# Kernel optimization log

Measured on AMD Instinct MI355X. Metric: run time of the kernel, lower is better.

## Reference

```python
import jax, jax.numpy as jnp
import numpy as np

B, C, H, W = 8, 96, 56, 56
N = H * W
K = 9
COUT = 2 * C  # 192


def setup_inputs() -> dict:
    key = jax.random.key(0)
    ks = jax.random.split(key, 12)
    s = 0.05
    inp = {
        "x": jax.random.normal(ks[0], (B, C, H, W), jnp.float32),
        "kmap_w": jax.random.normal(ks[1], (C, 500), jnp.float32) * s,
        "kmap_b": jnp.zeros((500,), jnp.float32),
        "kfc_w": jax.random.normal(ks[2], (500, 64), jnp.float32) * s,
        "kfc_b": jnp.zeros((64,), jnp.float32),
        "kmu_w": jax.random.normal(ks[3], (64, 32), jnp.float32) * s,
        "kmu_b": jnp.zeros((32,), jnp.float32),
        "kdec_w": jax.random.normal(ks[4], (32, K), jnp.float32) * s,
        "kdec_b": jnp.zeros((K,), jnp.float32),
        "ec1_w": jax.random.normal(ks[5], (2 * C, C), jnp.float32) * s,
        "ec1_b": jnp.zeros((C,), jnp.float32),
        "ec2_w": jax.random.normal(ks[6], (2 * C, C), jnp.float32) * s,
        "ec2_b": jnp.zeros((C,), jnp.float32),
        "fc_w": jax.random.normal(ks[7], (C, COUT), jnp.float32) * s,
        "fc_b": jnp.zeros((COUT,), jnp.float32),
        "io_w": jax.random.normal(ks[8], (C, COUT), jnp.float32) * s,
        "io_b": jnp.zeros((COUT,), jnp.float32),
        "up_w": jax.random.normal(ks[9], (2 * COUT, COUT), jnp.float32) * s,
        "up_b": jnp.zeros((COUT,), jnp.float32),
    }
    return inp


def reference(x, kmap_w, kmap_b, kfc_w, kfc_b, kmu_w, kmu_b, kdec_w, kdec_b,
              ec1_w, ec1_b, ec2_w, ec2_b, fc_w, fc_b, io_w, io_b, up_w, up_b):
    b, c, h, w = x.shape
    n = h * w
    xf = x.reshape(b, c, n).transpose(0, 2, 1)  # [B, N, C]

    # ---- dense kNN graph (dilation=1, deterministic) ----
    sq = jnp.sum(xf * xf, axis=-1)  # [B, N]
    dist = sq[:, :, None] - 2.0 * jnp.einsum('bnc,bmc->bnm', xf, xf) + sq[:, None, :]
    _, nn_idx = jax.lax.top_k(-dist, K)  # [B, N, K] local neighbor indices

    nodes = xf.reshape(b * n, c)  # flat node features

    # ---- VAE-like K predictor -> per-node kept-degree (non-differentiable) ----
    hK = nodes @ kmap_w + kmap_b
    hK = jax.nn.relu(hK @ kfc_w + kfc_b)
    mu = hK @ kmu_w + kmu_b
    logits = mu @ kdec_w + kdec_b  # [B*N, K]
    k_int = jnp.argmax(logits, axis=1)  # in [0, K-1]

    # edge mask: keep first k_int[i] of node i's K edges
    edge_mask = (jnp.arange(K)[None, :] < k_int[:, None]).reshape(-1)  # [B*N*K]
    emask = edge_mask.astype(nodes.dtype)[:, None]

    # flatten edges with per-batch node offsets (local -> global indices)
    offs = (jnp.arange(b) * n)[:, None, None]
    src = (nn_idx + offs).reshape(-1)              # x_j
    dst = jnp.repeat(jnp.arange(b * n), K)         # x_i (center)

    def edge_conv(feat, wgt, bias):
        xi = feat[dst]
        xj = feat[src]
        msg = jnp.concatenate([xi, xj - xi], axis=-1) @ wgt + bias
        msg = msg * emask  # pruned edges contribute 0 to 'add' aggregation
        return jax.ops.segment_sum(msg, dst, num_segments=b * n)

    h1 = jax.nn.relu(edge_conv(nodes, ec1_w, ec1_b))
    h2 = edge_conv(h1, ec2_w, ec2_b)
    agg = h2 @ fc_w + fc_b                 # EdgeAgg output [B*N, COUT]

    xio = nodes @ io_w + io_b              # inOutFC
    upd = jax.nn.relu(jnp.concatenate([xio, agg], axis=-1) @ up_w + up_b)

    out = upd.reshape(b, n, 2 * c).transpose(0, 2, 1).reshape(b, 2 * c, h, w)
    return out
```

## Files before the change

### kernel.cpp

```cpp
#include <hip/hip_runtime.h>

#define NODES 25088
#define NB 8
#define NPB 3136
#define C 96
#define KNN 9
#define COUT 192
#define MSPLIT 4
#define T12 12
#define NCAND (MSPLIT * T12)

typedef float f32x4 __attribute__((ext_vector_type(4)));
typedef float f32x16 __attribute__((ext_vector_type(16)));
typedef short s16x8 __attribute__((ext_vector_type(8)));

__device__ __forceinline__ unsigned short f2bf(float x) {
  unsigned u = __float_as_uint(x);
  return (unsigned short)((u + 0x7fffu + ((u >> 16) & 1u)) >> 16);
}
__device__ __forceinline__ float bf2f(unsigned short h) {
  return __uint_as_float(((unsigned)h) << 16);
}

__global__ __launch_bounds__(256) void txsq_kernel(
    const float* __restrict__ x, float* __restrict__ xf, float* __restrict__ sq,
    unsigned short* __restrict__ xh, unsigned short* __restrict__ xl) {
  __shared__ float t[96][33];
  int tid = threadIdx.x;
  int b = blockIdx.y;
  int n0 = blockIdx.x * 32;
  const float* xb = x + (size_t)b * C * NPB;
  int tn = tid & 31, tc = tid >> 5;
#pragma unroll
  for (int i = 0; i < 12; i++) {
    int c = tc + i * 8;
    t[c][tn] = xb[(size_t)c * NPB + n0 + tn];
  }
  __syncthreads();
#pragma unroll
  for (int k = 0; k < 3; k++) {
    int it = tid + k * 256;
    int nl = it / 24, c4 = it % 24;
    int node = b * NPB + n0 + nl;
    float4 v;
    v.x = t[4 * c4 + 0][nl];
    v.y = t[4 * c4 + 1][nl];
    v.z = t[4 * c4 + 2][nl];
    v.w = t[4 * c4 + 3][nl];
    ushort4 h, l;
    h.x = f2bf(v.x); l.x = f2bf(v.x - bf2f(h.x));
    h.y = f2bf(v.y); l.y = f2bf(v.y - bf2f(h.y));
    h.z = f2bf(v.z); l.z = f2bf(v.z - bf2f(h.z));
    h.w = f2bf(v.w); l.w = f2bf(v.w - bf2f(h.w));
    ((float4*)(xf + (size_t)node * C))[c4] = v;
    ((ushort4*)(xh + (size_t)node * C))[c4] = h;
    ((ushort4*)(xl + (size_t)node * C))[c4] = l;
  }
  if (tid < 32) {
    int node = b * NPB + n0 + tid;
    float s = 0.f;
#pragma unroll
    for (int i = 0; i < 24; i++) {
      float4 v;
      v.x = t[4 * i + 0][tid];
      v.y = t[4 * i + 1][tid];
      v.z = t[4 * i + 2][tid];
      v.w = t[4 * i + 3][tid];
      s += v.x * v.x + v.y * v.y + v.z * v.z + v.w * v.w;
    }
    sq[node] = s;
  }
}

__global__ void fold_all_kernel(
    const float* __restrict__ kmap_w, const float* __restrict__ kmap_b,
    const float* __restrict__ kfc_w, const float* __restrict__ kfc_b,
    const float* __restrict__ kmu_w, const float* __restrict__ kmu_b,
    const float* __restrict__ kdec_w, const float* __restrict__ kdec_b,
    const float* __restrict__ ec1_w, const float* __restrict__ ec2_w,
    const float* __restrict__ io_w, const float* __restrict__ io_b,
    const float* __restrict__ fc_w, const float* __restrict__ fc_b,
    const float* __restrict__ up_w, const float* __restrict__ up_b,
    float* __restrict__ WkP, float* __restrict__ bkP, float* __restrict__ WdP,
    float* __restrict__ bdP, float* __restrict__ bPf,
    unsigned short* __restrict__ B1h, unsigned short* __restrict__ B1l,
    unsigned short* __restrict__ B2h, unsigned short* __restrict__ B2l,
    unsigned short* __restrict__ BFh, unsigned short* __restrict__ BFl) {
  __shared__ float sh[4][64];
  int bid = blockIdx.x, tid = threadIdx.x;
  int tx = tid & 63, ty = tid >> 6;
  if (bid < 96) {
    int m = bid;
    float acc = 0.f;
    for (int k = ty; k < 500; k += 4) acc += kmap_w[m * 500 + k] * kfc_w[k * 64 + tx];
    sh[ty][tx] = acc;
    __syncthreads();
    if (ty == 0) WkP[m * 64 + tx] = sh[0][tx] + sh[1][tx] + sh[2][tx] + sh[3][tx];
  } else if (bid == 96) {
    float acc = 0.f;
    for (int k = ty; k < 500; k += 4) acc += kmap_b[k] * kfc_w[k * 64 + tx];
    sh[ty][tx] = acc;
    __syncthreads();
    if (ty == 0) bkP[tx] = sh[0][tx] + sh[1][tx] + sh[2][tx] + sh[3][tx] + kfc_b[tx];
  } else if (bid < 161) {
    int m = bid - 97;
    float acc = 0.f;
    if (tx < 9) {
      for (int k = ty; k < 32; k += 4) acc += kmu_w[m * 32 + k] * kdec_w[k * 9 + tx];
    }
    sh[ty][tx] = acc;
    __syncthreads();
    if (ty == 0 && tx < 9) WdP[m * 9 + tx] = sh[0][tx] + sh[1][tx] + sh[2][tx] + sh[3][tx];
  } else if (bid == 161) {
    float acc = 0.f;
    if (tx < 9) {
      for (int k = ty; k < 32; k += 4) acc += kmu_b[k] * kdec_w[k * 9 + tx];
    }
    sh[ty][tx] = acc;
    __syncthreads();
    if (ty == 0 && tx < 9) bdP[tx] = sh[0][tx] + sh[1][tx] + sh[2][tx] + sh[3][tx] + kdec_b[tx];
  } else if (bid < 234) {
    int t = (bid - 162) * 256 + tid;
    int n = t / 192, k = t % 192;
    float v = ec1_w[(size_t)k * 96 + n];
    if (k < 96) v -= ec1_w[(size_t)(k + 96) * 96 + n];
    unsigned short h = f2bf(v);
    B1h[t] = h;
    B1l[t] = f2bf(v - bf2f(h));
  } else if (bid < 306) {
    int t = (bid - 234) * 256 + tid;
    int n = t / 192, k = t % 192;
    float v = ec2_w[(size_t)k * 96 + n];
    if (k < 96) v -= ec2_w[(size_t)(k + 96) * 96 + n];
    unsigned short h = f2bf(v);
    B2h[t] = h;
    B2l[t] = f2bf(v - bf2f(h));
  } else if (bid < 594) {
    int r = bid - 306;
    int m = r / 3, n = (r % 3) * 64 + tx;
    float acc = 0.f;
    for (int k = ty; k < 192; k += 4) acc += io_w[m * 192 + k] * up_w[(size_t)k * 192 + n];
    sh[ty][tx] = acc;
    __syncthreads();
    if (ty == 0) {
      float v = sh[0][tx] + sh[1][tx] + sh[2][tx] + sh[3][tx];
      unsigned short h = f2bf(v);
      BFh[(size_t)n * 192 + m] = h;
      BFl[(size_t)n * 192 + m] = f2bf(v - bf2f(h));
    }
  } else if (bid < 882) {
    int r = bid - 594;
    int m = r / 3, n = (r % 3) * 64 + tx;
    float acc = 0.f;
    for (int k = ty; k < 192; k += 4)
      acc += fc_w[m * 192 + k] * up_w[(size_t)(192 + k) * 192 + n];
    sh[ty][tx] = acc;
    __syncthreads();
    if (ty == 0) {
      float v = sh[0][tx] + sh[1][tx] + sh[2][tx] + sh[3][tx];
      unsigned short h = f2bf(v);
      BFh[(size_t)n * 192 + 96 + m] = h;
      BFl[(size_t)n * 192 + 96 + m] = f2bf(v - bf2f(h));
    }
  } else {
    if (tid < 192) {
      float acc = up_b[tid];
      for (int k = 0; k < 192; k++) {
        acc += io_b[k] * up_w[k * 192 + tid];
        acc += fc_b[k] * up_w[(192 + k) * 192 + tid];
      }
      bPf[tid] = acc;
    }
  }
}

__global__ __launch_bounds__(256) void gemmhead_kernel(
    const float* __restrict__ A0, const float* __restrict__ B,
    const float* __restrict__ bias, const float* __restrict__ WdP,
    const float* __restrict__ bdP, int* __restrict__ kint,
    float* __restrict__ rs) {
  __shared__ float As[16][68];
  __shared__ float Bs[16][68];
  __shared__ float hs[64][68];
  __shared__ float wd[576];
  __shared__ float bd[9];
  int tid = threadIdx.x;
  int tx = tid & 15, ty = tid >> 4;
  int row0 = blockIdx.x * 64;
  for (int f = tid; f < 576; f += 256) wd[f] = WdP[f];
  if (tid < 9) bd[tid] = bdP[tid];
  float acc[4][4] = {};
  int ai = tid >> 2;
  int ak = (tid & 3) * 4;
  int bk = tid >> 4;
  int bj = (tid & 15) * 4;

  for (int k0 = 0; k0 < 96; k0 += 16) {
    {
      int r = row0 + ai;
      float4 v = *(const float4*)(A0 + (size_t)r * 96 + k0 + ak);
      As[ak + 0][ai] = v.x;
      As[ak + 1][ai] = v.y;
      As[ak + 2][ai] = v.z;
      As[ak + 3][ai] = v.w;
    }
    {
      int kg = k0 + bk;
      float4 v = *(const float4*)(B + (size_t)kg * 64 + bj);
      *(float4*)&Bs[bk][bj] = v;
    }
    __syncthreads();
#pragma unroll
    for (int kk = 0; kk < 16; kk++) {
      float4 av = *(const float4*)&As[kk][ty * 4];
      float4 bv = *(const float4*)&Bs[kk][tx * 4];
      acc[0][0] += av.x * bv.x; acc[0][1] += av.x * bv.y; acc[0][2] += av.x * bv.z; acc[0][3] += av.x * bv.w;
      acc[1][0] += av.y * bv.x; acc[1][1] += av.y * bv.y; acc[1][2] += av.y * bv.z; acc[1][3] += av.y * bv.w;
      acc[2][0] += av.z * bv.x; acc[2][1] += av.z * bv.y; acc[2][2] += av.z * bv.z; acc[2][3] += av.z * bv.w;
      acc[3][0] += av.w * bv.x; acc[3][1] += av.w * bv.y; acc[3][2] += av.w * bv.z; acc[3][3] += av.w * bv.w;
    }
    __syncthreads();
  }
#pragma unroll
  for (int ii = 0; ii < 4; ii++) {
#pragma unroll
    for (int jj = 0; jj < 4; jj++) {
      int j = tx * 4 + jj;
      hs[ty * 4 + ii][j] = fmaxf(acc[ii][jj] + bias[j], 0.f);
    }
  }
  __syncthreads();
  if (tid < 64) {
    int node = row0 + tid;
    const float4* hp = (const float4*)hs[tid];
    float4 h[16];
#pragma unroll
    for (int i = 0; i < 16; i++) h[i] = hp[i];
    float best = -3.4e38f;
    int bi = 0;
#pragma unroll
    for (int n = 0; n < 9; n++) {
      float a = bd[n];
#pragma unroll
      for (int k = 0; k < 16; k++) {
        float4 hv = h[k];
        a += hv.x * wd[(4 * k + 0) * 9 + n] + hv.y * wd[(4 * k + 1) * 9 + n] +
             hv.z * wd[(4 * k + 2) * 9 + n] + hv.w * wd[(4 * k + 3) * 9 + n];
      }
      if (a > best) { best = a; bi = n; }
    }
    kint[node] = bi;
    rs[node] = (float)bi;
  }
}

__device__ __forceinline__ void ce(float& a, float& b) {
  float lo = fminf(a, b);
  b = fmaxf(a, b);
  a = lo;
}

__device__ __forceinline__ void sort16(float* s) {
  ce(s[0], s[1]); ce(s[2], s[3]); ce(s[0], s[2]); ce(s[1], s[3]); ce(s[1], s[2]);
  ce(s[4], s[5]); ce(s[6], s[7]); ce(s[4], s[6]); ce(s[5], s[7]); ce(s[5], s[6]);
  ce(s[0], s[4]); ce(s[1], s[5]); ce(s[2], s[6]); ce(s[3], s[7]);
  ce(s[2], s[4]); ce(s[3], s[5]);
  ce(s[1], s[2]); ce(s[3], s[4]); ce(s[5], s[6]);
  ce(s[8], s[9]); ce(s[10], s[11]); ce(s[8], s[10]); ce(s[9], s[11]); ce(s[9], s[10]);
  ce(s[12], s[13]); ce(s[14], s[15]); ce(s[12], s[14]); ce(s[13], s[15]); ce(s[13], s[14]);
  ce(s[8], s[12]); ce(s[9], s[13]); ce(s[10], s[14]); ce(s[11], s[15]);
  ce(s[10], s[12]); ce(s[11], s[13]);
  ce(s[9], s[10]); ce(s[11], s[12]); ce(s[13], s[14]);
  ce(s[0], s[8]); ce(s[1], s[9]); ce(s[2], s[10]); ce(s[3], s[11]);
  ce(s[4], s[12]); ce(s[5], s[13]); ce(s[6], s[14]); ce(s[7], s[15]);
  ce(s[4], s[8]); ce(s[5], s[9]); ce(s[6], s[10]); ce(s[7], s[11]);
  ce(s[2], s[4]); ce(s[3], s[5]); ce(s[6], s[8]); ce(s[7], s[9]);
  ce(s[10], s[12]); ce(s[11], s[13]);
  ce(s[1], s[2]); ce(s[3], s[4]); ce(s[5], s[6]); ce(s[7], s[8]);
  ce(s[9], s[10]); ce(s[11], s[12]); ce(s[13], s[14]);
}

__device__ __forceinline__ void bmerge12(float* fd, const float* s) {
  float L[12];
#pragma unroll
  for (int i = 0; i < 12; i++) L[i] = fminf(fd[i], s[11 - i]);
  ce(L[0], L[8]); ce(L[1], L[9]); ce(L[2], L[10]); ce(L[3], L[11]);
  ce(L[4], L[8]); ce(L[5], L[9]); ce(L[6], L[10]); ce(L[7], L[11]);
  ce(L[0], L[2]); ce(L[1], L[3]); ce(L[4], L[6]); ce(L[5], L[7]);
  ce(L[8], L[10]); ce(L[9], L[11]);
  ce(L[0], L[1]); ce(L[2], L[3]); ce(L[4], L[5]); ce(L[6], L[7]);
  ce(L[8], L[9]); ce(L[10], L[11]);
#pragma unroll
  for (int i = 0; i < 12; i++) fd[i] = L[i];
}

__global__ __launch_bounds__(256) void knn_mfma_kernel(
    const unsigned short* __restrict__ xh, const unsigned short* __restrict__ xl,
    const float* __restrict__ sq, int* __restrict__ pk_i) {
  __shared__ __align__(16) float smem_f[6784];
  unsigned short* mhA = (unsigned short*)smem_f;
  unsigned short* mhB = (unsigned short*)(smem_f + 3328);
  float* sqsA = smem_f + 6656;
  float* sqsB = smem_f + 6720;
  int tid = threadIdx.x;
  int lane = tid & 63, wv = tid >> 6;
  int wm = wv >> 1, wq = wv & 1;
  int bid = blockIdx.x;
  int b = bid & 7;
  int r = bid >> 3;
  int q0 = (r % 49) * 64;
  int z = r / 49;
  int bbase = b * NPB;
  int t0 = (z * 49) / MSPLIT, t1 = ((z + 1) * 49) / MSPLIT;

  int koff = (lane >> 5) * 8;
  int qrow = bbase + q0 + wq * 32 + (lane & 31);
  s16x8 bqh[6], bql[6];
  {
    const unsigned short* ph = xh + (size_t)qrow * 96 + koff;
    const unsigned short* pl = xl + (size_t)qrow * 96 + koff;
#pragma unroll
    for (int kc = 0; kc < 6; kc++) {
      bqh[kc] = *(const s16x8*)(ph + kc * 16);
      bql[kc] = *(const s16x8*)(pl + kc * 16);
    }
  }
  float sqr = sq[qrow];

  float fd[12];
#pragma unroll
  for (int k = 0; k < 12; k++) fd[k] = 3.4e38f;

  int srow = tid >> 1;
  int tloc = srow >> 6;
  int rrow = srow & 63;
  int sseg = (tid & 1) * 48;
  int soff = rrow * 104 + sseg;
  unsigned short* mhd = tloc ? mhB : mhA;

  s16x8 st[6];
  float stq = 0.f;
  {
    int tA = t0 + tloc;
    int ts = (tA < t1) ? tA : (t1 - 1);
    const unsigned short* gh = xh + (size_t)(bbase + ts * 64 + rrow) * 96 + sseg;
#pragma unroll
    for (int i = 0; i < 6; i++) st[i] = *(const s16x8*)(gh + i * 8);
    if (tid < 128) {
      int tq = t0 + (tid >> 6);
      int tqs = (tq < t1) ? tq : (t1 - 1);
      stq = sq[bbase + tqs * 64 + (tid & 63)];
    }
  }

  int sqbase = wm * 32 + 4 * (lane >> 5);
  int mrow = wm * 32 + (lane & 31);
  int np = (t1 - t0 + 1) >> 1;

  for (int p = 0; p < np; p++) {
    int ta = t0 + 2 * p, tb = ta + 1;
    __syncthreads();
#pragma unroll
    for (int i = 0; i < 6; i++) *(s16x8*)(mhd + soff + i * 8) = st[i];
    if (tid < 128) ((tid >> 6) ? sqsB : sqsA)[tid & 63] = stq;
    __syncthreads();

    {
      int tn = t0 + 2 * (p + 1) + tloc;
      int ts = (tn < t1) ? tn : (t1 - 1);
      const unsigned short* gh = xh + (size_t)(bbase + ts * 64 + rrow) * 96 + sseg;
#pragma unroll
      for (int i = 0; i < 6; i++) st[i] = *(const s16x8*)(gh + i * 8);
      if (tid < 128) {
        int tq = t0 + 2 * (p + 1) + (tid >> 6);
        int tqs = (tq < t1) ? tq : (t1 - 1);
        stq = sq[bbase + tqs * 64 + (tid & 63)];
      }
    }

    {
      f32x16 acc = (f32x16){0.f, 0.f, 0.f, 0.f, 0.f, 0.f, 0.f, 0.f,
                            0.f, 0.f, 0.f, 0.f, 0.f, 0.f, 0.f, 0.f};
#pragma unroll
      for (int kc = 0; kc < 6; kc++) {
        s16x8 amh = *(const s16x8*)(mhA + mrow * 104 + kc * 16 + koff);
        acc = __builtin_amdgcn_mfma_f32_32x32x16_bf16(amh, bqh[kc], acc, 0, 0, 0);
        acc = __builtin_amdgcn_mfma_f32_32x32x16_bf16(amh, bql[kc], acc, 0, 0, 0);
      }
      f32x4 sm0 = *(const f32x4*)(sqsA + sqbase);
      f32x4 sm1 = *(const f32x4*)(sqsA + sqbase + 8);
      f32x4 sm2 = *(const f32x4*)(sqsA + sqbase + 16);
      f32x4 sm3 = *(const f32x4*)(sqsA + sqbase + 24);
      int lbase = (ta - t0) * 64;
      float cs[16];
#pragma unroll
      for (int reg = 0; reg < 16; reg++) {
        int g = reg >> 2, e = reg & 3;
        float sqm = (g == 0) ? sm0[e] : (g == 1) ? sm1[e] : (g == 2) ? sm2[e] : sm3[e];
        int mloc = wm * 32 + e + 8 * g + 4 * (lane >> 5);
        float d = fmaf(-2.f, acc[reg], sqr + sqm);
        unsigned u = (__float_as_uint(d) & 0xFFFFFC00u) | (unsigned)(lbase + mloc);
        cs[reg] = __uint_as_float(u);
      }
      sort16(cs);
      bmerge12(fd, cs);
    }
    if (tb < t1) {
      f32x16 acc = (f32x16){0.f, 0.f, 0.f, 0.f, 0.f, 0.f, 0.f, 0.f,
                            0.f, 0.f, 0.f, 0.f, 0.f, 0.f, 0.f, 0.f};
#pragma unroll
      for (int kc = 0; kc < 6; kc++) {
        s16x8 amh = *(const s16x8*)(mhB + mrow * 104 + kc * 16 + koff);
        acc = __builtin_amdgcn_mfma_f32_32x32x16_bf16(amh, bqh[kc], acc, 0, 0, 0);
        acc = __builtin_amdgcn_mfma_f32_32x32x16_bf16(amh, bql[kc], acc, 0, 0, 0);
      }
      f32x4 sm0 = *(const f32x4*)(sqsB + sqbase);
      f32x4 sm1 = *(const f32x4*)(sqsB + sqbase + 8);
      f32x4 sm2 = *(const f32x4*)(sqsB + sqbase + 16);
      f32x4 sm3 = *(const f32x4*)(sqsB + sqbase + 24);
      int lbase = (tb - t0) * 64;
      float cs[16];
#pragma unroll
      for (int reg = 0; reg < 16; reg++) {
        int g = reg >> 2, e = reg & 3;
        float sqm = (g == 0) ? sm0[e] : (g == 1) ? sm1[e] : (g == 2) ? sm2[e] : sm3[e];
        int mloc = wm * 32 + e + 8 * g + 4 * (lane >> 5);
        float d = fmaf(-2.f, acc[reg], sqr + sqm);
        unsigned u = (__float_as_uint(d) & 0xFFFFFC00u) | (unsigned)(lbase + mloc);
        cs[reg] = __uint_as_float(u);
      }
      sort16(cs);
      bmerge12(fd, cs);
    }
  }

  __syncthreads();
  float* cd = smem_f;
#pragma unroll
  for (int k = 0; k < 12; k++) cd[(wv * 64 + lane) * 13 + k] = fd[k];
  __syncthreads();
  if (wv == 0) {
    int wva = lane >> 5, ql = lane & 31;
    int ra = wva * 64 + ql, rb = wva * 64 + ql + 32;
    int rc = (wva + 2) * 64 + ql, rd = (wva + 2) * 64 + ql + 32;
    float A[12], B[12];
#pragma unroll
    for (int k = 0; k < 12; k++) { A[k] = cd[ra * 13 + k]; B[k] = cd[rb * 13 + k]; }
    bmerge12(A, B);
    float Cc[12], Dd[12];
#pragma unroll
    for (int k = 0; k < 12; k++) { Cc[k] = cd[rc * 13 + k]; Dd[k] = cd[rd * 13 + k]; }
    bmerge12(Cc, Dd);
    bmerge12(A, Cc);
    size_t base = ((size_t)(bbase + q0 + lane) * MSPLIT + z) * T12;
#pragma unroll
    for (int k = 0; k < T12; k++) {
      int mloc = (int)(__float_as_uint(A[k]) & 0x3FFu) + t0 * 64;
      pk_i[base + k] = bbase + mloc;
    }
  }
}

__global__ __launch_bounds__(256) void rescore_kernel(
    const float* __restrict__ xf, const float* __restrict__ sq,
    const int* __restrict__ pk_i, int* __restrict__ nn) {
  __shared__ float qr[4][96];
  __shared__ float sqq[4];
  int tid = threadIdx.x;
  int qloc = tid >> 6, c = tid & 63;
  int bid = blockIdx.x;
  int qbase = (bid & 7) * NPB + (bid >> 3) * 4;
  for (int f = tid; f < 4 * 96; f += 256)
    qr[f / 96][f % 96] = xf[(size_t)(qbase + f / 96) * 96 + f % 96];
  if (tid < 4) sqq[tid] = sq[qbase + tid];
  __syncthreads();

  int q = qbase + qloc;
  int jv = 0;
  if (c < NCAND) jv = pk_i[(size_t)q * NCAND + c];

  int grp = c >> 3;
  int chunk = c & 7;
  const float4* qp = (const float4*)qr[qloc];
  float4 qv0 = qp[chunk];
  float4 qv1 = qp[chunk + 8];
  float4 qv2 = qp[chunk + 16];

  float dots[6];
#pragma unroll
  for (int it = 0; it < 6; it++) {
    int j = __shfl(jv, it * 8 + grp, 64);
    const float4* mp = (const float4*)(xf + (size_t)j * 96);
    float4 m0 = mp[chunk];
    float4 m1 = mp[chunk + 8];
    float4 m2 = mp[chunk + 16];
    float p = qv0.x * m0.x + qv0.y * m0.y + qv0.z * m0.z + qv0.w * m0.w +
              qv1.x * m1.x + qv1.y * m1.y + qv1.z * m1.z + qv1.w * m1.w +
              qv2.x * m2.x + qv2.y * m2.y + qv2.z * m2.z + qv2.w * m2.w;
    p += __shfl_xor(p, 1, 64);
    p += __shfl_xor(p, 2, 64);
    p += __shfl_xor(p, 4, 64);
    dots[it] = p;
  }

  float g0 = __shfl(dots[0], (c & 7) * 8, 64);
  float g1 = __shfl(dots[1], (c & 7) * 8, 64);
  float g2 = __shfl(dots[2], (c & 7) * 8, 64);
  float g3 = __shfl(dots[3], (c & 7) * 8, 64);
  float g4 = __shfl(dots[4], (c & 7) * 8, 64);
  float g5 = __shfl(dots[5], (c & 7) * 8, 64);
  int itstar = c >> 3;
  float dot = g0;
  dot = (itstar == 1) ? g1 : dot;
  dot = (itstar == 2) ? g2 : dot;
  dot = (itstar == 3) ? g3 : dot;
  dot = (itstar == 4) ? g4 : dot;
  dot = (itstar == 5) ? g5 : dot;

  unsigned long long key = 0xFFFFFFFFFFFFFFFFull;
  if (c < NCAND) {
    float d = (sqq[qloc] - 2.0f * dot) + sq[jv];
    unsigned u = __float_as_uint(d);
    u ^= (u & 0x80000000u) ? 0xFFFFFFFFu : 0x80000000u;
    key = ((unsigned long long)u << 32) | (unsigned)jv;
  }

#pragma unroll
  for (int k = 2; k <= 64; k <<= 1) {
#pragma unroll
    for (int jm = k >> 1; jm >= 1; jm >>= 1) {
      unsigned long long other = __shfl_xor(key, jm, 64);
      bool takeMin = ((c & jm) == 0) == ((c & k) == 0);
      bool sw = (other < key) == takeMin;
      key = sw ? other : key;
    }
  }

  if (c < KNN) {
    nn[(size_t)q * KNN + c] = (int)(unsigned)(key & 0xFFFFFFFFull);
  }
}

// ... 139 lines not shown
    }
    size_t bo = (size_t)n * 192 + c * 16 + koff;
    s16x8 bh = *(const s16x8*)(Bth + bo);
    s16x8 bl = *(const s16x8*)(Btl + bo);
    acc = __builtin_amdgcn_mfma_f32_32x32x16_bf16(ah, bh, acc, 0, 0, 0);
    acc = __builtin_amdgcn_mfma_f32_32x32x16_bf16(al, bh, acc, 0, 0, 0);
    acc = __builtin_amdgcn_mfma_f32_32x32x16_bf16(ah, bl, acc, 0, 0, 0);
  }

  float bn = bL[wv * 32 + nloc];
#pragma unroll
  for (int reg = 0; reg < 16; reg++) {
    int rl = (reg & 3) + 8 * (reg >> 2) + 4 * (lane >> 5);
    tt[wv][nloc][rl] = fmaxf(acc[reg] + bn, 0.f);
  }
  __builtin_amdgcn_s_waitcnt(0);
  int gbase = m0 + nloc;
  int bb = gbase / NPB, nidx = gbase % NPB;
#pragma unroll
  for (int i = 0; i < 16; i++) {
    int nl = 2 * i + (lane >> 5);
    float v = tt[wv][nl][nloc];
    int ng = n0 + wv * 32 + nl;
    out[(size_t)bb * COUT * NPB + (size_t)ng * NPB + nidx] = v;
  }
}

extern "C" void kernel_launch(void* const* d_in, const int* in_sizes, int n_in,
                              void* d_out, int out_size, void* d_ws, size_t ws_size,
                              hipStream_t stream) {
  const float* x      = (const float*)d_in[0];
  const float* kmap_w = (const float*)d_in[1];
  const float* kmap_b = (const float*)d_in[2];
  const float* kfc_w  = (const float*)d_in[3];
  const float* kfc_b  = (const float*)d_in[4];
  const float* kmu_w  = (const float*)d_in[5];
  const float* kmu_b  = (const float*)d_in[6];
  const float* kdec_w = (const float*)d_in[7];
  const float* kdec_b = (const float*)d_in[8];
  const float* ec1_w  = (const float*)d_in[9];
  const float* ec1_b  = (const float*)d_in[10];
  const float* ec2_w  = (const float*)d_in[11];
  const float* ec2_b  = (const float*)d_in[12];
  const float* fc_w   = (const float*)d_in[13];
  const float* fc_b   = (const float*)d_in[14];
  const float* io_w   = (const float*)d_in[15];
  const float* io_b   = (const float*)d_in[16];
  const float* up_w   = (const float*)d_in[17];
  const float* up_b   = (const float*)d_in[18];

  char* ws = (char*)d_ws;
  size_t off = 0;
  auto alloc = [&](size_t bytes) -> void* {
    void* p = ws + off;
    off += (bytes + 255) & ~(size_t)255;
    return p;
  };
  const size_t HBF = (size_t)NODES * C * 2;
  float* xf   = (float*)alloc((size_t)NODES * C * 4);
  float* sqb  = (float*)alloc((size_t)NODES * 4);
  float* rs   = (float*)alloc((size_t)NODES * 4);
  int*   kint = (int*)alloc((size_t)NODES * 4);
  int*   nn   = (int*)alloc((size_t)NODES * KNN * 4);
  unsigned short* xh = (unsigned short*)alloc(HBF);
  unsigned short* xl = (unsigned short*)alloc(HBF);
  char* region = (char*)alloc((size_t)NODES * COUT * 4);
  int*   pk_i   = (int*)region;
  unsigned short* h1h = (unsigned short*)region;
  unsigned short* h1l = (unsigned short*)(region + HBF);
  unsigned short* h2h = (unsigned short*)(region + 2 * HBF);
  unsigned short* h2l = (unsigned short*)(region + 3 * HBF);
  float* WkP = (float*)alloc(96 * 64 * 4);
  float* bkP = (float*)alloc(64 * 4);
  float* WdP = (float*)alloc(64 * 9 * 4);
  float* bdP = (float*)alloc(16 * 4);
  float* bPf = (float*)alloc(192 * 4);
  unsigned short* B1h = (unsigned short*)alloc(96 * 192 * 2);
  unsigned short* B1l = (unsigned short*)alloc(96 * 192 * 2);
  unsigned short* B2h = (unsigned short*)alloc(96 * 192 * 2);
  unsigned short* B2l = (unsigned short*)alloc(96 * 192 * 2);
  unsigned short* BFh = (unsigned short*)alloc(192 * 192 * 2);
  unsigned short* BFl = (unsigned short*)alloc(192 * 192 * 2);

  txsq_kernel<<<dim3(98, 8), 256, 0, stream>>>(x, xf, sqb, xh, xl);

  fold_all_kernel<<<883, 256, 0, stream>>>(
      kmap_w, kmap_b, kfc_w, kfc_b, kmu_w, kmu_b, kdec_w, kdec_b, ec1_w, ec2_w,
      io_w, io_b, fc_w, fc_b, up_w, up_b,
      WkP, bkP, WdP, bdP, bPf, B1h, B1l, B2h, B2l, BFh, BFl);

  gemmhead_kernel<<<392, 256, 0, stream>>>(xf, WkP, bkP, WdP, bdP, kint, rs);

  knn_mfma_kernel<<<1568, 256, 0, stream>>>(xh, xl, sqb, pk_i);
  rescore_kernel<<<6272, 256, 0, stream>>>(xf, sqb, pk_i, nn);

  mfma_ec_fused_kernel<<<784, 192, 0, stream>>>(
      xh, xl, xf, (const unsigned short*)nullptr, (const unsigned short*)nullptr,
      0, nn, kint, B1h, B1l, rs, ec1_b, 1, h1h, h1l);
  mfma_ec_fused_kernel<<<784, 192, 0, stream>>>(
      h1h, h1l, (const float*)nullptr, h1h, h1l,
      1, nn, kint, B2h, B2l, rs, ec2_b, 0, h2h, h2l);
  mfma_final_kernel<<<dim3(784, 2), 192, 0, stream>>>(xh, xl, h2h, h2l, BFh, BFl,
                                                      bPf, (float*)d_out);
}
```

Measured before the change: 320.0 us.

## Merge independent kernels into two block-dispatched launches to cut launch overhead

Combines the transpose/split kernel with the weight-folding kernel into one launch, and the kNN MFMA kernel with the K-predictor GEMM head into another, choosing the role of each block by its block index. Independent work now runs concurrently within one grid, and two kernel launches and their inter-kernel gaps go away. In exchange, the fused kernels carry the union of shared-memory sizes and register pressure, which may reduce occupancy for the lighter branches.

```diff
diff --git a/kernel.cpp b/kernel.cpp
--- a/kernel.cpp
+++ b/kernel.cpp
@@ -22,57 +22,49 @@
   return __uint_as_float(((unsigned)h) << 16);
 }
 
-__global__ __launch_bounds__(256) void txsq_kernel(
+__device__ __forceinline__ void ce(float& a, float& b) {
+  float lo = fminf(a, b);
+  b = fmaxf(a, b);
+  a = lo;
+}
+
+__device__ __forceinline__ void sort16(float* s) {
+  ce(s[0], s[1]); ce(s[2], s[3]); ce(s[0], s[2]); ce(s[1], s[3]); ce(s[1], s[2]);
+  ce(s[4], s[5]); ce(s[6], s[7]); ce(s[4], s[6]); ce(s[5], s[7]); ce(s[5], s[6]);
+  ce(s[0], s[4]); ce(s[1], s[5]); ce(s[2], s[6]); ce(s[3], s[7]);
+  ce(s[2], s[4]); ce(s[3], s[5]);
+  ce(s[1], s[2]); ce(s[3], s[4]); ce(s[5], s[6]);
+  ce(s[8], s[9]); ce(s[10], s[11]); ce(s[8], s[10]); ce(s[9], s[11]); ce(s[9], s[10]);
+  ce(s[12], s[13]); ce(s[14], s[15]); ce(s[12], s[14]); ce(s[13], s[15]); ce(s[13], s[14]);
+  ce(s[8], s[12]); ce(s[9], s[13]); ce(s[10], s[14]); ce(s[11], s[15]);
+  ce(s[10], s[12]); ce(s[11], s[13]);
+  ce(s[9], s[10]); ce(s[11], s[12]); ce(s[13], s[14]);
+  ce(s[0], s[8]); ce(s[1], s[9]); ce(s[2], s[10]); ce(s[3], s[11]);
+  ce(s[4], s[12]); ce(s[5], s[13]); ce(s[6], s[14]); ce(s[7], s[15]);
+  ce(s[4], s[8]); ce(s[5], s[9]); ce(s[6], s[10]); ce(s[7], s[11]);
+  ce(s[2], s[4]); ce(s[3], s[5]); ce(s[6], s[8]); ce(s[7], s[9]);
+  ce(s[10], s[12]); ce(s[11], s[13]);
+  ce(s[1], s[2]); ce(s[3], s[4]); ce(s[5], s[6]); ce(s[7], s[8]);
+  ce(s[9], s[10]); ce(s[11], s[12]); ce(s[13], s[14]);
+}
+
+__device__ __forceinline__ void bmerge12(float* fd, const float* s) {
+  float L[12];
+#pragma unroll
+  for (int i = 0; i < 12; i++) L[i] = fminf(fd[i], s[11 - i]);
+  ce(L[0], L[8]); ce(L[1], L[9]); ce(L[2], L[10]); ce(L[3], L[11]);
+  ce(L[4], L[8]); ce(L[5], L[9]); ce(L[6], L[10]); ce(L[7], L[11]);
+  ce(L[0], L[2]); ce(L[1], L[3]); ce(L[4], L[6]); ce(L[5], L[7]);
+  ce(L[8], L[10]); ce(L[9], L[11]);
+  ce(L[0], L[1]); ce(L[2], L[3]); ce(L[4], L[5]); ce(L[6], L[7]);
+  ce(L[8], L[9]); ce(L[10], L[11]);
+#pragma unroll
+  for (int i = 0; i < 12; i++) fd[i] = L[i];
+}
+
+__global__ __launch_bounds__(256) void stage1_kernel(
     const float* __restrict__ x, float* __restrict__ xf, float* __restrict__ sq,
-    unsigned short* __restrict__ xh, unsigned short* __restrict__ xl) {
-  __shared__ float t[96][33];
-  int tid = threadIdx.x;
-  int b = blockIdx.y;
-  int n0 = blockIdx.x * 32;
-  const float* xb = x + (size_t)b * C * NPB;
-  int tn = tid & 31, tc = tid >> 5;
-#pragma unroll
-  for (int i = 0; i < 12; i++) {
-    int c = tc + i * 8;
-    t[c][tn] = xb[(size_t)c * NPB + n0 + tn];
-  }
-  __syncthreads();
-#pragma unroll
-  for (int k = 0; k < 3; k++) {
-    int it = tid + k * 256;
-    int nl = it / 24, c4 = it % 24;
-    int node = b * NPB + n0 + nl;
-    float4 v;
-    v.x = t[4 * c4 + 0][nl];
-    v.y = t[4 * c4 + 1][nl];
-    v.z = t[4 * c4 + 2][nl];
-    v.w = t[4 * c4 + 3][nl];
-    ushort4 h, l;
-    h.x = f2bf(v.x); l.x = f2bf(v.x - bf2f(h.x));
-    h.y = f2bf(v.y); l.y = f2bf(v.y - bf2f(h.y));
-    h.z = f2bf(v.z); l.z = f2bf(v.z - bf2f(h.z));
-    h.w = f2bf(v.w); l.w = f2bf(v.w - bf2f(h.w));
-    ((float4*)(xf + (size_t)node * C))[c4] = v;
-    ((ushort4*)(xh + (size_t)node * C))[c4] = h;
-    ((ushort4*)(xl + (size_t)node * C))[c4] = l;
-  }
-  if (tid < 32) {
-    int node = b * NPB + n0 + tid;
-    float s = 0.f;
-#pragma unroll
-    for (int i = 0; i < 24; i++) {
-      float4 v;
-      v.x = t[4 * i + 0][tid];
-      v.y = t[4 * i + 1][tid];
-      v.z = t[4 * i + 2][tid];
-      v.w = t[4 * i + 3][tid];
-      s += v.x * v.x + v.y * v.y + v.z * v.z + v.w * v.w;
-    }
-    sq[node] = s;
-  }
-}
-
-__global__ void fold_all_kernel(
+    unsigned short* __restrict__ xh, unsigned short* __restrict__ xl,
     const float* __restrict__ kmap_w, const float* __restrict__ kmap_b,
     const float* __restrict__ kfc_w, const float* __restrict__ kfc_b,
     const float* __restrict__ kmu_w, const float* __restrict__ kmu_b,
@@ -86,8 +78,57 @@
     unsigned short* __restrict__ B1h, unsigned short* __restrict__ B1l,
     unsigned short* __restrict__ B2h, unsigned short* __restrict__ B2l,
     unsigned short* __restrict__ BFh, unsigned short* __restrict__ BFl) {
-  __shared__ float sh[4][64];
-  int bid = blockIdx.x, tid = threadIdx.x;
+  __shared__ __align__(16) char smem[12672];
+  int gbid = blockIdx.x, tid = threadIdx.x;
+  if (gbid < 784) {
+    float (*t)[33] = (float(*)[33])smem;
+    int nt = gbid % 98, b = gbid / 98;
+    int n0 = nt * 32;
+    const float* xb = x + (size_t)b * C * NPB;
+    int tn = tid & 31, tc = tid >> 5;
+#pragma unroll
+    for (int i = 0; i < 12; i++) {
+      int c = tc + i * 8;
+      t[c][tn] = xb[(size_t)c * NPB + n0 + tn];
+    }
+    __syncthreads();
+#pragma unroll
+    for (int k = 0; k < 3; k++) {
+      int it = tid + k * 256;
+      int nl = it / 24, c4 = it % 24;
+      int node = b * NPB + n0 + nl;
+      float4 v;
+      v.x = t[4 * c4 + 0][nl];
+      v.y = t[4 * c4 + 1][nl];
+      v.z = t[4 * c4 + 2][nl];
+      v.w = t[4 * c4 + 3][nl];
+      ushort4 h, l;
+      h.x = f2bf(v.x); l.x = f2bf(v.x - bf2f(h.x));
+      h.y = f2bf(v.y); l.y = f2bf(v.y - bf2f(h.y));
+      h.z = f2bf(v.z); l.z = f2bf(v.z - bf2f(h.z));
+      h.w = f2bf(v.w); l.w = f2bf(v.w - bf2f(h.w));
+      ((float4*)(xf + (size_t)node * C))[c4] = v;
+      ((ushort4*)(xh + (size_t)node * C))[c4] = h;
+      ((ushort4*)(xl + (size_t)node * C))[c4] = l;
+    }
+    if (tid < 32) {
+      int node = b * NPB + n0 + tid;
+      float s = 0.f;
+#pragma unroll
+      for (int i = 0; i < 24; i++) {
+        float4 v;
+        v.x = t[4 * i + 0][tid];
+        v.y = t[4 * i + 1][tid];
+        v.z = t[4 * i + 2][tid];
+        v.w = t[4 * i + 3][tid];
+        s += v.x * v.x + v.y * v.y + v.z * v.z + v.w * v.w;
+      }
+      sq[node] = s;
+    }
+    return;
+  }
+  float (*sh)[64] = (float(*)[64])smem;
+  int bid = gbid - 784;
   int tx = tid & 63, ty = tid >> 6;
   if (bid < 96) {
     int m = bid;
@@ -174,19 +215,186 @@
   }
 }
 
-__global__ __launch_bounds__(256) void gemmhead_kernel(
+__global__ __launch_bounds__(256) void stage2_kernel(
+    const unsigned short* __restrict__ xh, const unsigned short* __restrict__ xl,
+    const float* __restrict__ sq, int* __restrict__ pk_i,
     const float* __restrict__ A0, const float* __restrict__ B,
     const float* __restrict__ bias, const float* __restrict__ WdP,
     const float* __restrict__ bdP, int* __restrict__ kint,
     float* __restrict__ rs) {
-  __shared__ float As[16][68];
-  __shared__ float Bs[16][68];
-  __shared__ float hs[64][68];
-  __shared__ float wd[576];
-  __shared__ float bd[9];
-  int tid = threadIdx.x;
+  __shared__ __align__(16) char smem[28464];
+  int gbid = blockIdx.x, tid = threadIdx.x;
+  if (gbid < 1568) {
+    float* smem_f = (float*)smem;
+    unsigned short* mhA = (unsigned short*)smem_f;
+    unsigned short* mhB = (unsigned short*)(smem_f + 3328);
+    float* sqsA = smem_f + 6656;
+    float* sqsB = smem_f + 6720;
+    int lane = tid & 63, wv = tid >> 6;
+    int wm = wv >> 1, wq = wv & 1;
+    int bid = gbid;
+    int b = bid & 7;
+    int r = bid >> 3;
+    int q0 = (r % 49) * 64;
+    int z = r / 49;
+    int bbase = b * NPB;
+    int t0 = (z * 49) / MSPLIT, t1 = ((z + 1) * 49) / MSPLIT;
+
+    int koff = (lane >> 5) * 8;
+    int qrow = bbase + q0 + wq * 32 + (lane & 31);
+    s16x8 bqh[6], bql[6];
+    {
+      const unsigned short* ph = xh + (size_t)qrow * 96 + koff;
+      const unsigned short* pl = xl + (size_t)qrow * 96 + koff;
+#pragma unroll
+      for (int kc = 0; kc < 6; kc++) {
+        bqh[kc] = *(const s16x8*)(ph + kc * 16);
+        bql[kc] = *(const s16x8*)(pl + kc * 16);
+      }
+    }
+    float sqr = sq[qrow];
+
+    float fd[12];
+#pragma unroll
+    for (int k = 0; k < 12; k++) fd[k] = 3.4e38f;
+
+    int srow = tid >> 1;
+    int tloc = srow >> 6;
+    int rrow = srow & 63;
+    int sseg = (tid & 1) * 48;
+    int soff = rrow * 104 + sseg;
+    unsigned short* mhd = tloc ? mhB : mhA;
+
+    s16x8 st[6];
+    float stq = 0.f;
+    {
+      int tA = t0 + tloc;
+      int ts = (tA < t1) ? tA : (t1 - 1);
+      const unsigned short* gh = xh + (size_t)(bbase + ts * 64 + rrow) * 96 + sseg;
+#pragma unroll
+      for (int i = 0; i < 6; i++) st[i] = *(const s16x8*)(gh + i * 8);
+      if (tid < 128) {
+        int tq = t0 + (tid >> 6);
+        int tqs = (tq < t1) ? tq : (t1 - 1);
+        stq = sq[bbase + tqs * 64 + (tid & 63)];
+      }
+    }
+
+    int sqbase = wm * 32 + 4 * (lane >> 5);
+    int mrow = wm * 32 + (lane & 31);
+    int np = (t1 - t0 + 1) >> 1;
+
+    for (int p = 0; p < np; p++) {
+      int ta = t0 + 2 * p, tb = ta + 1;
+      __syncthreads();
+#pragma unroll
+      for (int i = 0; i < 6; i++) *(s16x8*)(mhd + soff + i * 8) = st[i];
+      if (tid < 128) ((tid >> 6) ? sqsB : sqsA)[tid & 63] = stq;
+      __syncthreads();
+
+      {
+        int tn = t0 + 2 * (p + 1) + tloc;
+        int ts = (tn < t1) ? tn : (t1 - 1);
+        const unsigned short* gh = xh + (size_t)(bbase + ts * 64 + rrow) * 96 + sseg;
+#pragma unroll
+        for (int i = 0; i < 6; i++) st[i] = *(const s16x8*)(gh + i * 8);
+        if (tid < 128) {
+          int tq = t0 + 2 * (p + 1) + (tid >> 6);
+          int tqs = (tq < t1) ? tq : (t1 - 1);
+          stq = sq[bbase + tqs * 64 + (tid & 63)];
+        }
+      }
+
+      {
+        f32x16 acc = (f32x16){0.f, 0.f, 0.f, 0.f, 0.f, 0.f, 0.f, 0.f,
+                              0.f, 0.f, 0.f, 0.f, 0.f, 0.f, 0.f, 0.f};
+#pragma unroll
+        for (int kc = 0; kc < 6; kc++) {
+          s16x8 amh = *(const s16x8*)(mhA + mrow * 104 + kc * 16 + koff);
+          acc = __builtin_amdgcn_mfma_f32_32x32x16_bf16(amh, bqh[kc], acc, 0, 0, 0);
+          acc = __builtin_amdgcn_mfma_f32_32x32x16_bf16(amh, bql[kc], acc, 0, 0, 0);
+        }
+        f32x4 sm0 = *(const f32x4*)(sqsA + sqbase);
+        f32x4 sm1 = *(const f32x4*)(sqsA + sqbase + 8);
+        f32x4 sm2 = *(const f32x4*)(sqsA + sqbase + 16);
+        f32x4 sm3 = *(const f32x4*)(sqsA + sqbase + 24);
+        int lbase = (ta - t0) * 64;
+        float cs[16];
+#pragma unroll
+        for (int reg = 0; reg < 16; reg++) {
+          int g = reg >> 2, e = reg & 3;
+          float sqm = (g == 0) ? sm0[e] : (g == 1) ? sm1[e] : (g == 2) ? sm2[e] : sm3[e];
+          int mloc = wm * 32 + e + 8 * g + 4 * (lane >> 5);
+          float d = fmaf(-2.f, acc[reg], sqr + sqm);
+          unsigned u = (__float_as_uint(d) & 0xFFFFFC00u) | (unsigned)(lbase + mloc);
+          cs[reg] = __uint_as_float(u);
+        }
+        sort16(cs);
+        bmerge12(fd, cs);
+      }
+      if (tb < t1) {
+        f32x16 acc = (f32x16){0.f, 0.f, 0.f, 0.f, 0.f, 0.f, 0.f, 0.f,
+                              0.f, 0.f, 0.f, 0.f, 0.f, 0.f, 0.f, 0.f};
+#pragma unroll
+        for (int kc = 0; kc < 6; kc++) {
+          s16x8 amh = *(const s16x8*)(mhB + mrow * 104 + kc * 16 + koff);
+          acc = __builtin_amdgcn_mfma_f32_32x32x16_bf16(amh, bqh[kc], acc, 0, 0, 0);
+          acc = __builtin_amdgcn_mfma_f32_32x32x16_bf16(amh, bql[kc], acc, 0, 0, 0);
+        }
+        f32x4 sm0 = *(const f32x4*)(sqsB + sqbase);
+        f32x4 sm1 = *(const f32x4*)(sqsB + sqbase + 8);
+        f32x4 sm2 = *(const f32x4*)(sqsB + sqbase + 16);
+        f32x4 sm3 = *(const f32x4*)(sqsB + sqbase + 24);
+        int lbase = (tb - t0) * 64;
+        float cs[16];
+#pragma unroll
+        for (int reg = 0; reg < 16; reg++) {
+          int g = reg >> 2, e = reg & 3;
+          float sqm = (g == 0) ? sm0[e] : (g == 1) ? sm1[e] : (g == 2) ? sm2[e] : sm3[e];
+          int mloc = wm * 32 + e + 8 * g + 4 * (lane >> 5);
+          float d = fmaf(-2.f, acc[reg], sqr + sqm);
+          unsigned u = (__float_as_uint(d) & 0xFFFFFC00u) | (unsigned)(lbase + mloc);
+          cs[reg] = __uint_as_float(u);
+        }
+        sort16(cs);
+        bmerge12(fd, cs);
+      }
+    }
+
+    __syncthreads();
+    float* cd = smem_f;
+#pragma unroll
+    for (int k = 0; k < 12; k++) cd[(wv * 64 + lane) * 13 + k] = fd[k];
+    __syncthreads();
+    if (wv == 0) {
+      int wva = lane >> 5, ql = lane & 31;
+      int ra = wva * 64 + ql, rb = wva * 64 + ql + 32;
+      int rc = (wva + 2) * 64 + ql, rd = (wva + 2) * 64 + ql + 32;
+      float A[12], Bb[12];
+#pragma unroll
+      for (int k = 0; k < 12; k++) { A[k] = cd[ra * 13 + k]; Bb[k] = cd[rb * 13 + k]; }
+      bmerge12(A, Bb);
+      float Cc[12], Dd[12];
+#pragma unroll
+      for (int k = 0; k < 12; k++) { Cc[k] = cd[rc * 13 + k]; Dd[k] = cd[rd * 13 + k]; }
+      bmerge12(Cc, Dd);
+      bmerge12(A, Cc);
+      size_t base = ((size_t)(bbase + q0 + lane) * MSPLIT + z) * T12;
+#pragma unroll
+      for (int k = 0; k < T12; k++) {
+        int mloc = (int)(__float_as_uint(A[k]) & 0x3FFu) + t0 * 64;
+        pk_i[base + k] = bbase + mloc;
+      }
+    }
+    return;
+  }
+  float (*As)[68] = (float(*)[68])(smem);
+  float (*Bs)[68] = (float(*)[68])(smem + 4352);
+  float (*hs)[68] = (float(*)[68])(smem + 8704);
+  float* wd = (float*)(smem + 26112);
+  float* bd = (float*)(smem + 28416);
   int tx = tid & 15, ty = tid >> 4;
-  int row0 = blockIdx.x * 64;
+  int row0 = (gbid - 1568) * 64;
   for (int f = tid; f < 576; f += 256) wd[f] = WdP[f];
   if (tid < 9) bd[tid] = bdP[tid];
   float acc[4][4] = {};
@@ -251,213 +459,6 @@
     }
     kint[node] = bi;
     rs[node] = (float)bi;
-  }
-}
-
-__device__ __forceinline__ void ce(float& a, float& b) {
-  float lo = fminf(a, b);
-  b = fmaxf(a, b);
-  a = lo;
-}
-
-__device__ __forceinline__ void sort16(float* s) {
-  ce(s[0], s[1]); ce(s[2], s[3]); ce(s[0], s[2]); ce(s[1], s[3]); ce(s[1], s[2]);
-  ce(s[4], s[5]); ce(s[6], s[7]); ce(s[4], s[6]); ce(s[5], s[7]); ce(s[5], s[6]);
-  ce(s[0], s[4]); ce(s[1], s[5]); ce(s[2], s[6]); ce(s[3], s[7]);
-  ce(s[2], s[4]); ce(s[3], s[5]);
-  ce(s[1], s[2]); ce(s[3], s[4]); ce(s[5], s[6]);
-  ce(s[8], s[9]); ce(s[10], s[11]); ce(s[8], s[10]); ce(s[9], s[11]); ce(s[9], s[10]);
-  ce(s[12], s[13]); ce(s[14], s[15]); ce(s[12], s[14]); ce(s[13], s[15]); ce(s[13], s[14]);
-  ce(s[8], s[12]); ce(s[9], s[13]); ce(s[10], s[14]); ce(s[11], s[15]);
-  ce(s[10], s[12]); ce(s[11], s[13]);
-  ce(s[9], s[10]); ce(s[11], s[12]); ce(s[13], s[14]);
-  ce(s[0], s[8]); ce(s[1], s[9]); ce(s[2], s[10]); ce(s[3], s[11]);
-  ce(s[4], s[12]); ce(s[5], s[13]); ce(s[6], s[14]); ce(s[7], s[15]);
-  ce(s[4], s[8]); ce(s[5], s[9]); ce(s[6], s[10]); ce(s[7], s[11]);
-  ce(s[2], s[4]); ce(s[3], s[5]); ce(s[6], s[8]); ce(s[7], s[9]);
-  ce(s[10], s[12]); ce(s[11], s[13]);
-  ce(s[1], s[2]); ce(s[3], s[4]); ce(s[5], s[6]); ce(s[7], s[8]);
-  ce(s[9], s[10]); ce(s[11], s[12]); ce(s[13], s[14]);
-}
-
-__device__ __forceinline__ void bmerge12(float* fd, const float* s) {
-  float L[12];
-#pragma unroll
-  for (int i = 0; i < 12; i++) L[i] = fminf(fd[i], s[11 - i]);
-  ce(L[0], L[8]); ce(L[1], L[9]); ce(L[2], L[10]); ce(L[3], L[11]);
-  ce(L[4], L[8]); ce(L[5], L[9]); ce(L[6], L[10]); ce(L[7], L[11]);
-  ce(L[0], L[2]); ce(L[1], L[3]); ce(L[4], L[6]); ce(L[5], L[7]);
-  ce(L[8], L[10]); ce(L[9], L[11]);
-  ce(L[0], L[1]); ce(L[2], L[3]); ce(L[4], L[5]); ce(L[6], L[7]);
-  ce(L[8], L[9]); ce(L[10], L[11]);
-#pragma unroll
-  for (int i = 0; i < 12; i++) fd[i] = L[i];
-}
-
-__global__ __launch_bounds__(256) void knn_mfma_kernel(
-    const unsigned short* __restrict__ xh, const unsigned short* __restrict__ xl,
-    const float* __restrict__ sq, int* __restrict__ pk_i) {
-  __shared__ __align__(16) float smem_f[6784];
-  unsigned short* mhA = (unsigned short*)smem_f;
-  unsigned short* mhB = (unsigned short*)(smem_f + 3328);
-  float* sqsA = smem_f + 6656;
-  float* sqsB = smem_f + 6720;
-  int tid = threadIdx.x;
-  int lane = tid & 63, wv = tid >> 6;
-  int wm = wv >> 1, wq = wv & 1;
-  int bid = blockIdx.x;
-  int b = bid & 7;
-  int r = bid >> 3;
-  int q0 = (r % 49) * 64;
-  int z = r / 49;
-  int bbase = b * NPB;
-  int t0 = (z * 49) / MSPLIT, t1 = ((z + 1) * 49) / MSPLIT;
-
-  int koff = (lane >> 5) * 8;
-  int qrow = bbase + q0 + wq * 32 + (lane & 31);
-  s16x8 bqh[6], bql[6];
-  {
-    const unsigned short* ph = xh + (size_t)qrow * 96 + koff;
-    const unsigned short* pl = xl + (size_t)qrow * 96 + koff;
-#pragma unroll
-    for (int kc = 0; kc < 6; kc++) {
-      bqh[kc] = *(const s16x8*)(ph + kc * 16);
-      bql[kc] = *(const s16x8*)(pl + kc * 16);
-    }
-  }
-  float sqr = sq[qrow];
-
-  float fd[12];
-#pragma unroll
-  for (int k = 0; k < 12; k++) fd[k] = 3.4e38f;
-
-  int srow = tid >> 1;
-  int tloc = srow >> 6;
-  int rrow = srow & 63;
-  int sseg = (tid & 1) * 48;
-  int soff = rrow * 104 + sseg;
-  unsigned short* mhd = tloc ? mhB : mhA;
-
-  s16x8 st[6];
-  float stq = 0.f;
-  {
-    int tA = t0 + tloc;
-    int ts = (tA < t1) ? tA : (t1 - 1);
-    const unsigned short* gh = xh + (size_t)(bbase + ts * 64 + rrow) * 96 + sseg;
-#pragma unroll
-    for (int i = 0; i < 6; i++) st[i] = *(const s16x8*)(gh + i * 8);
-    if (tid < 128) {
-      int tq = t0 + (tid >> 6);
-      int tqs = (tq < t1) ? tq : (t1 - 1);
-      stq = sq[bbase + tqs * 64 + (tid & 63)];
-    }
-  }
-
-  int sqbase = wm * 32 + 4 * (lane >> 5);
-  int mrow = wm * 32 + (lane & 31);
-  int np = (t1 - t0 + 1) >> 1;
-
-  for (int p = 0; p < np; p++) {
-    int ta = t0 + 2 * p, tb = ta + 1;
-    __syncthreads();
-#pragma unroll
-    for (int i = 0; i < 6; i++) *(s16x8*)(mhd + soff + i * 8) = st[i];
-    if (tid < 128) ((tid >> 6) ? sqsB : sqsA)[tid & 63] = stq;
-    __syncthreads();
-
-    {
-      int tn = t0 + 2 * (p + 1) + tloc;
-      int ts = (tn < t1) ? tn : (t1 - 1);
-      const unsigned short* gh = xh + (size_t)(bbase + ts * 64 + rrow) * 96 + sseg;
-#pragma unroll
-      for (int i = 0; i < 6; i++) st[i] = *(const s16x8*)(gh + i * 8);
-      if (tid < 128) {
-        int tq = t0 + 2 * (p + 1) + (tid >> 6);
-        int tqs = (tq < t1) ? tq : (t1 - 1);
-        stq = sq[bbase + tqs * 64 + (tid & 63)];
-      }
-    }
-
-    {
-      f32x16 acc = (f32x16){0.f, 0.f, 0.f, 0.f, 0.f, 0.f, 0.f, 0.f,
-                            0.f, 0.f, 0.f, 0.f, 0.f, 0.f, 0.f, 0.f};
-#pragma unroll
-      for (int kc = 0; kc < 6; kc++) {
-        s16x8 amh = *(const s16x8*)(mhA + mrow * 104 + kc * 16 + koff);
-        acc = __builtin_amdgcn_mfma_f32_32x32x16_bf16(amh, bqh[kc], acc, 0, 0, 0);
-        acc = __builtin_amdgcn_mfma_f32_32x32x16_bf16(amh, bql[kc], acc, 0, 0, 0);
-      }
-      f32x4 sm0 = *(const f32x4*)(sqsA + sqbase);
-      f32x4 sm1 = *(const f32x4*)(sqsA + sqbase + 8);
-      f32x4 sm2 = *(const f32x4*)(sqsA + sqbase + 16);
-      f32x4 sm3 = *(const f32x4*)(sqsA + sqbase + 24);
-      int lbase = (ta - t0) * 64;
-      float cs[16];
-#pragma unroll
-      for (int reg = 0; reg < 16; reg++) {
-        int g = reg >> 2, e = reg & 3;
-        float sqm = (g == 0) ? sm0[e] : (g == 1) ? sm1[e] : (g == 2) ? sm2[e] : sm3[e];
-        int mloc = wm * 32 + e + 8 * g + 4 * (lane >> 5);
-        float d = fmaf(-2.f, acc[reg], sqr + sqm);
-        unsigned u = (__float_as_uint(d) & 0xFFFFFC00u) | (unsigned)(lbase + mloc);
-        cs[reg] = __uint_as_float(u);
-      }
-      sort16(cs);
-      bmerge12(fd, cs);
-    }
-    if (tb < t1) {
-      f32x16 acc = (f32x16){0.f, 0.f, 0.f, 0.f, 0.f, 0.f, 0.f, 0.f,
-                            0.f, 0.f, 0.f, 0.f, 0.f, 0.f, 0.f, 0.f};
-#pragma unroll
-      for (int kc = 0; kc < 6; kc++) {
-        s16x8 amh = *(const s16x8*)(mhB + mrow * 104 + kc * 16 + koff);
-        acc = __builtin_amdgcn_mfma_f32_32x32x16_bf16(amh, bqh[kc], acc, 0, 0, 0);
-        acc = __builtin_amdgcn_mfma_f32_32x32x16_bf16(amh, bql[kc], acc, 0, 0, 0);
-      }
-      f32x4 sm0 = *(const f32x4*)(sqsB + sqbase);
-      f32x4 sm1 = *(const f32x4*)(sqsB + sqbase + 8);
-      f32x4 sm2 = *(const f32x4*)(sqsB + sqbase + 16);
-      f32x4 sm3 = *(const f32x4*)(sqsB + sqbase + 24);
-      int lbase = (tb - t0) * 64;
-      float cs[16];
-#pragma unroll
-      for (int reg = 0; reg < 16; reg++) {
-        int g = reg >> 2, e = reg & 3;
-        float sqm = (g == 0) ? sm0[e] : (g == 1) ? sm1[e] : (g == 2) ? sm2[e] : sm3[e];
-        int mloc = wm * 32 + e + 8 * g + 4 * (lane >> 5);
-        float d = fmaf(-2.f, acc[reg], sqr + sqm);
-        unsigned u = (__float_as_uint(d) & 0xFFFFFC00u) | (unsigned)(lbase + mloc);
-        cs[reg] = __uint_as_float(u);
-      }
-      sort16(cs);
-      bmerge12(fd, cs);
-    }
-  }
-
-  __syncthreads();
-  float* cd = smem_f;
-#pragma unroll
-  for (int k = 0; k < 12; k++) cd[(wv * 64 + lane) * 13 + k] = fd[k];
-  __syncthreads();
-  if (wv == 0) {
-    int wva = lane >> 5, ql = lane & 31;
-    int ra = wva * 64 + ql, rb = wva * 64 + ql + 32;
-    int rc = (wva + 2) * 64 + ql, rd = (wva + 2) * 64 + ql + 32;
-    float A[12], B[12];
-#pragma unroll
-    for (int k = 0; k < 12; k++) { A[k] = cd[ra * 13 + k]; B[k] = cd[rb * 13 + k]; }
-    bmerge12(A, B);
-    float Cc[12], Dd[12];
-#pragma unroll
-    for (int k = 0; k < 12; k++) { Cc[k] = cd[rc * 13 + k]; Dd[k] = cd[rd * 13 + k]; }
-    bmerge12(Cc, Dd);
-    bmerge12(A, Cc);
-    size_t base = ((size_t)(bbase + q0 + lane) * MSPLIT + z) * T12;
-#pragma unroll
-    for (int k = 0; k < T12; k++) {
-      int mloc = (int)(__float_as_uint(A[k]) & 0x3FFu) + t0 * 64;
-      pk_i[base + k] = bbase + mloc;
-    }
   }
 }
 
@@ -763,16 +764,15 @@
   unsigned short* BFh = (unsigned short*)alloc(192 * 192 * 2);
   unsigned short* BFl = (unsigned short*)alloc(192 * 192 * 2);
 
-  txsq_kernel<<<dim3(98, 8), 256, 0, stream>>>(x, xf, sqb, xh, xl);
-
-  fold_all_kernel<<<883, 256, 0, stream>>>(
+  stage1_kernel<<<1667, 256, 0, stream>>>(
+      x, xf, sqb, xh, xl,
       kmap_w, kmap_b, kfc_w, kfc_b, kmu_w, kmu_b, kdec_w, kdec_b, ec1_w, ec2_w,
       io_w, io_b, fc_w, fc_b, up_w, up_b,
       WkP, bkP, WdP, bdP, bPf, B1h, B1l, B2h, B2l, BFh, BFl);
 
-  gemmhead_kernel<<<392, 256, 0, stream>>>(xf, WkP, bkP, WdP, bdP, kint, rs);
-
-  knn_mfma_kernel<<<1568, 256, 0, stream>>>(xh, xl, sqb, pk_i);
+  stage2_kernel<<<1960, 256, 0, stream>>>(
+      xh, xl, sqb, pk_i, xf, WkP, bkP, WdP, bdP, kint, rs);
+
   rescore_kernel<<<6272, 256, 0, stream>>>(xf, sqb, pk_i, nn);
 
   mfma_ec_fused_kernel<<<784, 192, 0, stream>>>(
```

New measurement: 333.0 us. 1.04x slower.
